# Kernel optimization log

Hardware: AMD Instinct MI355X
Metric: run time of the kernel (lower is better)

Reference implementation:

```python
import jax, jax.numpy as jnp
import numpy as np

# Config (matches BlockConfig defaults for linear attention)
B, S, D = 2, 4096, 2048
H, KVH, HD, CK = 16, 8, 128, 4   # n_heads, n_kv_heads, head_dim, conv_kernel
DQK, DV = KVH * HD, H * HD       # 1024, 2048
EPS = 1e-6


def setup_inputs() -> dict:
    key = jax.random.key(0)
    ks = jax.random.split(key, 12)
    std = 0.02
    return {
        "x": jax.random.normal(ks[0], (B, S, D), jnp.float32),
        "wq": jax.random.normal(ks[1], (DQK, D), jnp.float32) * std,
        "wk": jax.random.normal(ks[2], (DQK, D), jnp.float32) * std,
        "wv": jax.random.normal(ks[3], (DV, D), jnp.float32) * std,
        "wo": jax.random.normal(ks[4], (D, DV), jnp.float32) * std,
        "q_conv_w": jax.random.normal(ks[5], (DQK, 1, CK), jnp.float32) * std,
        "k_conv_w": jax.random.normal(ks[6], (DQK, 1, CK), jnp.float32) * std,
        "alpha_w": jax.random.normal(ks[7], (H, D), jnp.float32) * std,
        "alpha_b": jnp.zeros((H,), jnp.float32),
        "beta_w": jax.random.normal(ks[8], (H, D), jnp.float32) * std,
        "beta_b": jnp.zeros((H,), jnp.float32),
        "g_w": jax.random.normal(ks[9], (DV, D), jnp.float32) * std,
        "norm_q_w": jnp.ones((HD,), jnp.float32),
        "norm_k_w": jnp.ones((HD,), jnp.float32),
    }


def _rmsnorm(x, w):
    # normalize over last dim (head_dim) in fp32, elementwise affine, no bias
    xf = x.astype(jnp.float32)
    var = jnp.mean(xf * xf, axis=-1, keepdims=True)
    return (w * xf * jax.lax.rsqrt(var + EPS)).astype(x.dtype)


def _causal_dwconv(x, w):
    # x: (B, S, C); w: (C, 1, k) depthwise; torch Conv1d padding=k-1 then [:S]
    # == left-pad (k-1, 0) cross-correlation
    y = jax.lax.conv_general_dilated(
        x.transpose(0, 2, 1), w, window_strides=(1,),
        padding=[(CK - 1, 0)], feature_group_count=w.shape[0],
        dimension_numbers=("NCH", "OIH", "NCH"))
    return y.transpose(0, 2, 1)


def reference(x, wq, wk, wv, wo, q_conv_w, k_conv_w,
              alpha_w, alpha_b, beta_w, beta_b, g_w, norm_q_w, norm_k_w):
    Q = x @ wq.T                              # (B,S,DQK)
    K = x @ wk.T                              # (B,S,DQK)
    V = x @ wv.T                              # (B,S,DV)
    Q = _causal_dwconv(Q, q_conv_w)
    K = _causal_dwconv(K, k_conv_w)
    Q = _rmsnorm(Q.reshape(B, S, KVH, HD), norm_q_w)
    K = _rmsnorm(K.reshape(B, S, KVH, HD), norm_k_w)
    V = V.reshape(B, S, H, HD)
    alpha = jax.nn.sigmoid(x @ alpha_w.T + alpha_b)              # (B,S,H)
    beta = jax.nn.sigmoid(x @ beta_w.T + beta_b) / (HD ** 0.5)   # (B,S,H)
    rep = H // KVH
    Q = jnp.repeat(Q, rep, axis=2)            # (B,S,H,HD)
    K = jnp.repeat(K, rep, axis=2)

    # time-major for scan
    Qt = Q.transpose(1, 0, 2, 3)
    Kt = K.transpose(1, 0, 2, 3)
    Vt = V.transpose(1, 0, 2, 3)
    at = alpha.transpose(1, 0, 2)
    bt = beta.transpose(1, 0, 2)

    S0 = jnp.zeros((B, H, HD, HD), x.dtype)

    def step(S_state, inp):
        q_t, k_t, v_t, a_t, b_t = inp
        pred = jnp.einsum("bhd,bhdv->bhv", k_t, S_state)
        delta = v_t - pred
        update = jnp.einsum("bhv,bhd->bhdv", delta, k_t)
        S_state = a_t[:, :, None, None] * S_state + b_t[:, :, None, None] * update
        o_t = jnp.einsum("bhd,bhdv->bhv", q_t, S_state)
        return S_state, o_t

    _, O = jax.lax.scan(step, S0, (Qt, Kt, Vt, at, bt))  # O: (S,B,H,HD)
    out = O.transpose(1, 0, 2, 3).reshape(B, S, DV)
    g = jax.nn.sigmoid(x @ g_w.T)
    return (g * out) @ wo.T
```

## Files before the change

### kernel.cpp

```cpp
#include <hip/hip_runtime.h>
#include <stdint.h>

#define DEV static __device__ __forceinline__

typedef __bf16 bf16x8 __attribute__((ext_vector_type(8)));
typedef float f32x4 __attribute__((ext_vector_type(4)));

constexpr int Bc = 2, Sc = 4096, Dc = 2048, Hc = 16, KVHc = 8, HDc = 128;
constexpr int DQKc = 1024, DVc = 2048;
constexpr int Mc = Bc * Sc;
constexpr int NCATc = 6144;
constexpr int CT = 64;
constexpr int NCH = Sc / CT;
constexpr int COEF_STRIDE = 25088;
constexpr float EPSc = 1e-6f;

DEV uint16_t f2bf(float f) {
  uint32_t u = __float_as_uint(f);
  u += 0x7FFFu + ((u >> 16) & 1u);
  return (uint16_t)(u >> 16);
}
DEV float bf2f(uint16_t h) { return __uint_as_float(((uint32_t)h) << 16); }
DEV float sigmoidf_(float z) { return 1.0f / (1.0f + __expf(-z)); }

DEV void gload16(void* lds, const void* g) {
  auto gp = (const __attribute__((address_space(1))) uint32_t*)(uintptr_t)g;
  auto lp = (__attribute__((address_space(3))) uint32_t*)(uint32_t)(uintptr_t)lds;
  __builtin_amdgcn_global_load_lds(gp, lp, 16, 0, 0);
}

DEV void sync_lds() {
  asm volatile("s_waitcnt lgkmcnt(0)" ::: "memory");
  __builtin_amdgcn_sched_barrier(0);
  __builtin_amdgcn_s_barrier();
  __builtin_amdgcn_sched_barrier(0);
}

__global__ __launch_bounds__(256) void cast_kernel(const float* __restrict__ src,
                                                   uint16_t* __restrict__ dst, int n4) {
  int i = blockIdx.x * blockDim.x + threadIdx.x;
  int stride = gridDim.x * blockDim.x;
  for (; i < n4; i += stride) {
    float4 v = *(const float4*)(src + (size_t)i * 4);
    ushort4 o;
    o.x = f2bf(v.x); o.y = f2bf(v.y); o.z = f2bf(v.z); o.w = f2bf(v.w);
    *(ushort4*)(dst + (size_t)i * 4) = o;
  }
}

template <typename OutT>
__global__ __launch_bounds__(512, 2) void gemm256_bt(const uint16_t* __restrict__ A,
                                                     const uint16_t* __restrict__ Bw,
                                                     OutT* __restrict__ C, int Ndim, int Kdim,
                                                     int lda) {
  __shared__ uint16_t sT[2][2][2][8192];

  const int nbn = Ndim / 256;
  const int nwg = gridDim.x;
  int q = nwg >> 3, r = nwg & 7;
  int xcd = blockIdx.x & 7, lin = blockIdx.x >> 3;
  int swz = (xcd < r ? xcd * (q + 1) : r * (q + 1) + (xcd - r) * q) + lin;
  const int bm = swz / nbn, bn = swz % nbn;

  const int tid = threadIdx.x;
  const int wid = tid >> 6, lane = tid & 63;
  const int wm = wid >> 2, wn = wid & 3;
  const int lr = lane & 15;
  const int sswz8 = (((lane >> 4) ^ ((lr >> 1) & 3)) * 8);
  const int arow_base = wm * 128 + lr;
  const int brow_base = wn * 64 + lr;

  const uint16_t* Ab = A + (size_t)(bm * 256) * lda;
  const uint16_t* Bb = Bw + (size_t)(bn * 256) * Kdim;
  const int NT = Kdim >> 6;

  int srowA[2];
  int soff[2];
  const int wbase = tid & ~63;
#pragma unroll
  for (int u = 0; u < 2; ++u) {
    int L = u * 512 + tid;
    srowA[u] = L >> 2;
    soff[u] = (((L & 3) ^ ((L >> 3) & 3)) * 8);
  }

  auto STAGE = [&](int buf, int mat, int kh, int kt) {
    const uint16_t* gb = mat == 0 ? Ab : Bb;
    const int ld = mat == 0 ? lda : Kdim;
    uint16_t* rg = &sT[buf][mat][kh][0];
#pragma unroll
    for (int u = 0; u < 2; ++u) {
      const uint16_t* g = gb + (size_t)srowA[u] * ld + kt * 64 + kh * 32 + soff[u];
      gload16(rg + (u * 512 + wbase) * 8, g);
    }
  };

  f32x4 acc[8][4] = {};
  bf16x8 bfr[4];

  STAGE(0, 0, 0, 0); STAGE(0, 1, 0, 0);
  STAGE(0, 0, 1, 0); STAGE(0, 1, 1, 0);
  STAGE(1, 0, 0, 1); STAGE(1, 1, 0, 1);
  asm volatile("s_waitcnt vmcnt(4)" ::: "memory");
  __builtin_amdgcn_s_barrier();

  for (int kt = 0; kt < NT; ++kt) {
    const int buf = kt & 1;
    const uint16_t* aR0 = &sT[buf][0][0][0];
    const uint16_t* bR0 = &sT[buf][1][0][0];
    const uint16_t* aR1 = &sT[buf][0][1][0];
    const uint16_t* bR1 = &sT[buf][1][1][0];

    {
      bf16x8 af[4];
#pragma unroll
      for (int m = 0; m < 4; ++m)
        af[m] = *(const bf16x8*)&aR0[(arow_base + m * 16) * 32 + sswz8];
#pragma unroll
      for (int n = 0; n < 4; ++n)
        bfr[n] = *(const bf16x8*)&bR0[(brow_base + n * 16) * 32 + sswz8];
      if (kt + 1 < NT) STAGE(buf ^ 1, 0, 1, kt + 1);
      __builtin_amdgcn_s_setprio(1);
#pragma unroll
      for (int m = 0; m < 4; ++m)
#pragma unroll
        for (int n = 0; n < 4; ++n)
          acc[m][n] = __builtin_amdgcn_mfma_f32_16x16x32_bf16(af[m], bfr[n], acc[m][n], 0, 0, 0);
      __builtin_amdgcn_s_setprio(0);
      __builtin_amdgcn_s_barrier();
    }
    {
      bf16x8 af[4];
#pragma unroll
      for (int m = 0; m < 4; ++m)
        af[m] = *(const bf16x8*)&aR0[(arow_base + (m + 4) * 16) * 32 + sswz8];
      if (kt + 1 < NT) STAGE(buf ^ 1, 1, 1, kt + 1);
      __builtin_amdgcn_s_setprio(1);
#pragma unroll
      for (int m = 0; m < 4; ++m)
#pragma unroll
        for (int n = 0; n < 4; ++n)
          acc[m + 4][n] = __builtin_amdgcn_mfma_f32_16x16x32_bf16(af[m], bfr[n], acc[m + 4][n], 0, 0, 0);
      __builtin_amdgcn_s_setprio(0);
      __builtin_amdgcn_s_barrier();
    }
    {
      bf16x8 af[4];
#pragma unroll
      for (int m = 0; m < 4; ++m)
        af[m] = *(const bf16x8*)&aR1[(arow_base + m * 16) * 32 + sswz8];
#pragma unroll
      for (int n = 0; n < 4; ++n)
        bfr[n] = *(const bf16x8*)&bR1[(brow_base + n * 16) * 32 + sswz8];
      if (kt + 2 < NT) STAGE(buf, 0, 0, kt + 2);
      __builtin_amdgcn_s_setprio(1);
#pragma unroll
      for (int m = 0; m < 4; ++m)
#pragma unroll
        for (int n = 0; n < 4; ++n)
          acc[m][n] = __builtin_amdgcn_mfma_f32_16x16x32_bf16(af[m], bfr[n], acc[m][n], 0, 0, 0);
      __builtin_amdgcn_s_setprio(0);
      __builtin_amdgcn_s_barrier();
    }
    {
      bf16x8 af[4];
#pragma unroll
      for (int m = 0; m < 4; ++m)
        af[m] = *(const bf16x8*)&aR1[(arow_base + (m + 4) * 16) * 32 + sswz8];
      if (kt + 2 < NT) STAGE(buf, 1, 0, kt + 2);
      __builtin_amdgcn_s_setprio(1);
#pragma unroll
      for (int m = 0; m < 4; ++m)
#pragma unroll
        for (int n = 0; n < 4; ++n)
          acc[m + 4][n] = __builtin_amdgcn_mfma_f32_16x16x32_bf16(af[m], bfr[n], acc[m + 4][n], 0, 0, 0);
      __builtin_amdgcn_s_setprio(0);
    }
    if (kt + 1 < NT) {
      if (kt + 2 < NT)
        asm volatile("s_waitcnt vmcnt(4)" ::: "memory");
      else
        asm volatile("s_waitcnt vmcnt(0)" ::: "memory");
      __builtin_amdgcn_s_barrier();
    }
  }

  const int r0 = (lane >> 4) * 4;
#pragma unroll
  for (int m = 0; m < 8; ++m)
#pragma unroll
    for (int n = 0; n < 4; ++n) {
      int col = bn * 256 + wn * 64 + n * 16 + lr;
#pragma unroll
      for (int j = 0; j < 4; ++j) {
        int row = bm * 256 + wm * 128 + m * 16 + r0 + j;
        float val = acc[m][n][j];
        if constexpr (sizeof(OutT) == 2)
          C[(size_t)row * Ndim + col] = (OutT)f2bf(val);
        else
          C[(size_t)row * Ndim + col] = (OutT)val;
      }
    }
}

__global__ __launch_bounds__(256) void alphabeta_kernel(const float* __restrict__ x,
                                                        const float* __restrict__ aw,
                                                        const float* __restrict__ abias,
                                                        const float* __restrict__ bw,
                                                        const float* __restrict__ bbias,
                                                        float* __restrict__ out) {
  __shared__ float xs[4 * Dc];
  const int row0 = blockIdx.x * 4;
  const float* xp = x + (size_t)row0 * Dc;
  for (int i = threadIdx.x; i < 4 * Dc / 4; i += 256)
    *(float4*)&xs[i * 4] = *(const float4*)(xp + (size_t)i * 4);
  __syncthreads();
  const int o = threadIdx.x >> 3, lg = threadIdx.x & 7;
  const float* wrow = (o < 16) ? (aw + (size_t)o * Dc) : (bw + (size_t)(o - 16) * Dc);
  float s0 = 0.f, s1 = 0.f, s2 = 0.f, s3 = 0.f;
  for (int k = lg * 4; k < Dc; k += 32) {
    float4 wv = *(const float4*)(wrow + k);
    float4 x0 = *(const float4*)&xs[k];
    float4 x1 = *(const float4*)&xs[Dc + k];
    float4 x2 = *(const float4*)&xs[2 * Dc + k];
    float4 x3 = *(const float4*)&xs[3 * Dc + k];
    s0 += x0.x * wv.x + x0.y * wv.y + x0.z * wv.z + x0.w * wv.w;
    s1 += x1.x * wv.x + x1.y * wv.y + x1.z * wv.z + x1.w * wv.w;
    s2 += x2.x * wv.x + x2.y * wv.y + x2.z * wv.z + x2.w * wv.w;
    s3 += x3.x * wv.x + x3.y * wv.y + x3.z * wv.z + x3.w * wv.w;
  }
#pragma unroll
  for (int m = 1; m < 8; m <<= 1) {
    s0 += __shfl_xor(s0, m); s1 += __shfl_xor(s1, m);
    s2 += __shfl_xor(s2, m); s3 += __shfl_xor(s3, m);
  }
  if (lg == 0) {
    float bias = (o < 16) ? abias[o] : bbias[o - 16];
    float scale = (o >= 16) ? 0.08838834764831845f : 1.0f;
    out[(size_t)(row0 + 0) * 32 + o] = sigmoidf_(s0 + bias) * scale;
    out[(size_t)(row0 + 1) * 32 + o] = sigmoidf_(s1 + bias) * scale;
    out[(size_t)(row0 + 2) * 32 + o] = sigmoidf_(s2 + bias) * scale;
    out[(size_t)(row0 + 3) * 32 + o] = sigmoidf_(s3 + bias) * scale;
  }
}

__global__ __launch_bounds__(256) void convnorm_kernel(const uint16_t* __restrict__ C1,
                                                       const float* __restrict__ qcw,
                                                       const float* __restrict__ kcw,
                                                       const float* __restrict__ nqw,
                                                       const float* __restrict__ nkw,
                                                       uint16_t* __restrict__ Qn,
                                                       uint16_t* __restrict__ Kn) {
  const int wid = blockIdx.x * 4 + (threadIdx.x >> 6);
  const int lane = threadIdx.x & 63;
  const int kvh = wid & 7;
  const int t = (wid >> 3) & (Sc - 1);
  const int b = wid >> 15;
  float qv[2], kv[2];
#pragma unroll
  for (int half = 0; half < 2; ++half) {
    const int c = lane + half * 64;
    const int ch = kvh * HDc + c;
    float qs = 0.f, ks = 0.f;
#pragma unroll
    for (int j = 0; j < 4; ++j) {
      int tt = t - 3 + j;
      if (tt >= 0) {
        size_t rb = (size_t)(b * Sc + tt) * NCATc;
        qs = fmaf(bf2f(C1[rb + ch]), qcw[ch * 4 + j], qs);
        ks = fmaf(bf2f(C1[rb + 1024 + ch]), kcw[ch * 4 + j], ks);
      }
    }
    qv[half] = qs; kv[half] = ks;
  }
  float sq = qv[0] * qv[0] + qv[1] * qv[1];
  float sk = kv[0] * kv[0] + kv[1] * kv[1];
#pragma unroll
  for (int m = 1; m < 64; m <<= 1) { sq += __shfl_xor(sq, m); sk += __shfl_xor(sk, m); }
  const float rq = rsqrtf(sq * (1.f / HDc) + EPSc);
  const float rk = rsqrtf(sk * (1.f / HDc) + EPSc);
#pragma unroll
  for (int half = 0; half < 2; ++half) {
    const int c = lane + half * 64;
    size_t oidx = (size_t)(b * Sc + t) * DQKc + kvh * HDc + c;
    Qn[oidx] = f2bf(nqw[c] * qv[half] * rq);
    Kn[oidx] = f2bf(nkw[c] * kv[half] * rk);
  }
}

__global__ __launch_bounds__(256) void scores_kernel(const uint16_t* __restrict__ Qn,
                                                     const uint16_t* __restrict__ Kn,
                                                     const float* __restrict__ ab,
                                                     uint8_t* __restrict__ coef) {
  __shared__ __align__(16) char smem[137728];
  uint16_t* sK = (uint16_t*)smem;
  uint16_t* sQ = (uint16_t*)(smem + 17408);
  uint16_t* sF = (uint16_t*)smem;
  uint16_t* sM2 = (uint16_t*)(smem + 18432);
  float* Lb = (float*)(smem + 108544);
  float* bbv = Lb + 128;
  uint16_t* Ktg = (uint16_t*)(smem + 109568);
  uint16_t* Et = (uint16_t*)(smem + 128000);
  float* gCb = (float*)(smem + 137216);

  auto Wt_p  = [&](int hd) { return (float*)(smem + hd * 17408); };
  auto Msh_p = [&](int hd) { return (uint16_t*)(smem + 34816 + hd * 18432); };
  auto Msl_p = [&](int hd) { return (uint16_t*)(smem + 44032 + hd * 18432); };
  auto Thh_p = [&](int hd) { return (uint16_t*)(smem + 71680 + hd * 18432); };
  auto Thl_p = [&](int hd) { return (uint16_t*)(smem + 80896 + hd * 18432); };

  const int bid = blockIdx.x;
  const int c = bid & 63, kh = (bid >> 6) & 7, b = bid >> 9;
  const int t0 = c * 64;
  const int tid = threadIdx.x;
  const int w = tid >> 6, l = tid & 63, lr = l & 15, lk = (l >> 4) * 8;
  const int sr = tid >> 2, sq2 = tid & 3;

  auto cb_p = [&](int hd) {
    return coef + (size_t)((b * Hc + kh * 2 + hd) * NCH + c) * COEF_STRIDE;
  };

  {
    const size_t rb = (size_t)(b * Sc + t0 + sr) * DQKc + kh * HDc + sq2 * 32;
#pragma unroll
    for (int u = 0; u < 4; ++u) {
      uint4 kv = *(const uint4*)(Kn + rb + u * 8);
      uint4 qv = *(const uint4*)(Qn + rb + u * 8);
      *(uint4*)&sK[sr * 136 + sq2 * 32 + u * 8] = kv;
      *(uint4*)&sQ[sr * 136 + sq2 * 32 + u * 8] = qv;
    }
  }
  if (tid < 128) {
    const int hd = tid >> 6, tt = tid & 63;
    const float* abp = ab + (size_t)(b * Sc + t0 + tt) * 32 + (kh * 2 + hd);
    float av = fmaxf(abp[0], 1e-30f);
    float bv = abp[16];
    float la = log2f(av);
    float L = la;
#pragma unroll
    for (int off = 1; off < 64; off <<= 1) {
      float up = __shfl_up(L, off, 64);
      if (tt >= off) L += up;
    }
    Lb[hd * 64 + tt] = L; bbv[hd * 64 + tt] = bv;
    float* gout = (float*)(cb_p(hd) + 24576);
    gout[tt] = exp2f(L - la);
    gout[64 + tt] = exp2f(L);
  }
  __syncthreads();

  f32x4 kkacc[4] = {}, qkacc[4] = {};
#pragma unroll
  for (int k0 = 0; k0 < 128; k0 += 32) {
    bf16x8 ka = *(const bf16x8*)&sK[(16 * w + lr) * 136 + k0 + lk];
    bf16x8 qa = *(const bf16x8*)&sQ[(16 * w + lr) * 136 + k0 + lk];
#pragma unroll
    for (int n = 0; n < 4; ++n) {
      bf16x8 kb = *(const bf16x8*)&sK[(16 * n + lr) * 136 + k0 + lk];
      kkacc[n] = __builtin_amdgcn_mfma_f32_16x16x32_bf16(ka, kb, kkacc[n], 0, 0, 0);
      qkacc[n] = __builtin_amdgcn_mfma_f32_16x16x32_bf16(qa, kb, qkacc[n], 0, 0, 0);
    }
  }
  __syncthreads();

  {
#pragma unroll
    for (int u = 0; u < 4; ++u) {
      uint4 kd = *(const uint4*)&sK[sr * 136 + sq2 * 32 + u * 8];
      const int c0 = sq2 * 32 + u * 8;
      const int tsw = sr ^ (sq2 << 4);
      uint32_t x0 = kd.x, x1 = kd.y, x2 = kd.z, x3 = kd.w;
      Ktg[(c0 + 0) * 72 + tsw] = (uint16_t)x0; Ktg[(c0 + 1) * 72 + tsw] = (uint16_t)(x0 >> 16);
      Ktg[(c0 + 2) * 72 + tsw] = (uint16_t)x1; Ktg[(c0 + 3) * 72 + tsw] = (uint16_t)(x1 >> 16);
      Ktg[(c0 + 4) * 72 + tsw] = (uint16_t)x2; Ktg[(c0 + 5) * 72 + tsw] = (uint16_t)(x2 >> 16);
      Ktg[(c0 + 6) * 72 + tsw] = (uint16_t)x3; Ktg[(c0 + 7) * 72 + tsw] = (uint16_t)(x3 >> 16);
    }
    if (tid < 128) {
      const int hd = tid >> 6, tt = tid & 63;
      gCb[hd * 64 + tt] = exp2f(Lb[hd * 64 + 63] - Lb[hd * 64 + tt]) * bbv[hd * 64 + tt];
    }
  }
  __syncthreads();

#pragma unroll
  for (int hd = 0; hd < 2; ++hd) {
    float* Wt = Wt_p(hd);
    uint16_t* Mh = Msh_p(hd);
    uint16_t* Ml = Msl_p(hd);
    const float* Lh = Lb + hd * 64;
    const float* bh = bbv + hd * 64;
#pragma unroll
    for (int n = 0; n < 4; ++n)
#pragma unroll
      for (int jj = 0; jj < 4; ++jj) {
        const int i = 16 * w + (l >> 4) * 4 + jj;
        const int j = 16 * n + lr;
        float Li = Lh[i];
        float Lim = (i > 0) ? Lh[(i > 0) ? i - 1 : 0] : 0.f;
        float Lj = Lh[j];
        float bj = bh[j];
        float wv = (j < i) ? exp2f(Lim - Lj) * bj * kkacc[n][jj] : 0.f;
        Wt[j * 68 + i] = wv;
        float ms = (j <= i) ? exp2f(Li - Lj) * bj * qkacc[n][jj] : 0.f;
        uint16_t mh = f2bf(ms);
        Mh[i * 72 + j] = mh;
        Ml[i * 72 + j] = f2bf(ms - bf2f(mh));
      }
  }
  __syncthreads();

  if (tid < 128) {
    const int hd = tid >> 6, col = tid & 63;
    float* Wt = Wt_p(hd);
    uint16_t* Th = Thh_p(hd);
    uint16_t* Tl = Thl_p(hd);
    float acc[64];
#pragma unroll
    for (int i = 0; i < 64; ++i) acc[i] = 0.f;
#pragma unroll
    for (int ll = 0; ll < 64; ++ll) {
      float xl = ((col == ll) ? 1.f : 0.f) - acc[ll];
      uint16_t xh = f2bf(xl);
      Th[col * 72 + ll] = xh;
      Tl[col * 72 + ll] = f2bf(xl - bf2f(xh));
#pragma unroll
      for (int i = ll + 1; i < 64; ++i)
        acc[i] = fmaf(Wt[ll * 68 + i], xl, acc[i]);
    }
  }
  __syncthreads();

  for (int hd = 0; hd < 2; ++hd) {
    uint16_t* Mh = Msh_p(hd);
    uint16_t* Ml = Msl_p(hd);
    uint16_t* Th = Thh_p(hd);
    uint16_t* Tl = Thl_p(hd);
    uint16_t* m2out = (uint16_t*)cb_p(hd);
    uint16_t* fout = (uint16_t*)cb_p(hd) + 4096;

    {
      const int j2 = tid >> 2, tq = tid & 3;
#pragma unroll
      for (int p = 0; p < 16; ++p) {
        int t1 = tq * 16 + p;
        float ev = gCb[hd * 64 + t1] * (bf2f(Th[j2 * 72 + t1]) + bf2f(Tl[j2 * 72 + t1]));
        Et[j2 * 72 + t1] = f2bf(ev);
      }
    }
    __syncthreads();

    f32x4 m2acc[4] = {};
#pragma unroll
    for (int k0 = 0; k0 < 64; k0 += 32) {
      bf16x8 ah = *(const bf16x8*)&Mh[(16 * w + lr) * 72 + k0 + lk];
      bf16x8 al = *(const bf16x8*)&Ml[(16 * w + lr) * 72 + k0 + lk];
#pragma unroll
      for (int n = 0; n < 4; ++n) {
        bf16x8 bhf = *(const bf16x8*)&Th[(16 * n + lr) * 72 + k0 + lk];
        bf16x8 blf = *(const bf16x8*)&Tl[(16 * n + lr) * 72 + k0 + lk];
        m2acc[n] = __builtin_amdgcn_mfma_f32_16x16x32_bf16(ah, bhf, m2acc[n], 0, 0, 0);
        m2acc[n] = __builtin_amdgcn_mfma_f32_16x16x32_bf16(ah, blf, m2acc[n], 0, 0, 0);
        m2acc[n] = __builtin_amdgcn_mfma_f32_16x16x32_bf16(al, bhf, m2acc[n], 0, 0, 0);
      }
    }
    f32x4 facc[2][4] = {};
#pragma unroll
    for (int k0 = 0; k0 < 64; k0 += 32) {
      bf16x8 eb[4];
#pragma unroll
      for (int n = 0; n < 4; ++n)
        eb[n] = *(const bf16x8*)&Et[(16 * n + lr) * 72 + k0 + lk];
      const int ksw = (k0 + lk) ^ (w << 4);
      bf16x8 ka0 = *(const bf16x8*)&Ktg[(32 * w + lr) * 72 + ksw];
      bf16x8 ka1 = *(const bf16x8*)&Ktg[(32 * w + 16 + lr) * 72 + ksw];
#pragma unroll
      for (int n = 0; n < 4; ++n) {
        facc[0][n] = __builtin_amdgcn_mfma_f32_16x16x32_bf16(ka0, eb[n], facc[0][n], 0, 0, 0);
        facc[1][n] = __builtin_amdgcn_mfma_f32_16x16x32_bf16(ka1, eb[n], facc[1][n], 0, 0, 0);
      }
    }
#pragma unroll
    for (int n = 0; n < 4; ++n)
#pragma unroll
      for (int jj = 0; jj < 4; ++jj) {
        const int i = 16 * w + (l >> 4) * 4 + jj;
        const int j = 16 * n + lr;
        sM2[i * 72 + j] = f2bf(m2acc[n][jj]);
        sF[(32 * w + (l >> 4) * 4 + jj) * 72 + j] = f2bf(facc[0][n][jj]);
        sF[(32 * w + 16 + (l >> 4) * 4 + jj) * 72 + j] = f2bf(facc[1][n][jj]);
      }
    __syncthreads();
    {
      const int i2 = tid >> 2, tq = tid & 3;
      uint4 a0 = *(const uint4*)&sM2[i2 * 72 + tq * 16];
      uint4 a1 = *(const uint4*)&sM2[i2 * 72 + tq * 16 + 8];
      *(uint4*)(m2out + i2 * 64 + tq * 16) = a0;
      *(uint4*)(m2out + i2 * 64 + tq * 16 + 8) = a1;
#pragma unroll
      for (int e = 0; e < 4; ++e) {
        int L = tid * 4 + e;
        int rw = L >> 3, cu = (L & 7) * 8;
        *(uint4*)(fout + rw * 64 + cu) = *(const uint4*)&sF[rw * 72 + cu];
      }
    }
    __syncthreads();
  }
}

__global__ __launch_bounds__(256) void scan_kernel(const uint16_t* __restrict__ Qn,
                                                   const uint16_t* __restrict__ Kn,
                                                   uint16_t* C1,
                                                   const uint8_t* __restrict__ coef) {
  __shared__ __align__(16) uint16_t Kb[64 * 136];
  __shared__ __align__(16) uint16_t Qb[64 * 136];
  __shared__ __align__(16) uint16_t M2b[64 * 72];
  __shared__ __align__(16) uint16_t Fb[128 * 72];
  __shared__ __align__(16) uint16_t Vb[64 * 24];
  __shared__ __align__(16) uint16_t Rt[16 * 72];
  __shared__ __align__(16) uint16_t Sh[16 * 136];
  __shared__ __align__(16) uint16_t Slo[16 * 136];
  __shared__ float gABb[128];

  const int bid = blockIdx.x;
  const int kh = bid & 7;
  const int j2 = bid >> 3;
  const int sl = j2 >> 2;
  const int b = (j2 >> 1) & 1;
  const int h = kh * 2 + (j2 & 1);
  const int ch0 = (b * Hc + h) * NCH;

  const int tid = threadIdx.x;
  const int w = tid >> 6, l = tid & 63;
  const int lr = l & 15, lk = (l >> 4) * 8;
  const int row0 = 16 * w + (l >> 4) * 4;
  const int vcol = lr;
  const int sr = tid >> 2, sq2 = tid & 3;

  const size_t kqbase = (size_t)(b * Sc) * DQKc + kh * HDc;
  const size_t vbase = (size_t)(b * Sc) * NCATc + 2048 + h * HDc + sl * 16;
  uint16_t* Gb = C1 + (size_t)(b * Sc) * NCATc + 4096 + h * HDc + sl * 16 + vcol;

  float sreg[2][4] = {};
  uint4 kA[4], kB[4], qA[4], qB[4];
  ushort4 gv0, gv1;

  auto LOADS = [&](int cn, uint4 (&kd)[4], uint4 (&qd)[4], uint4 (&m2d)[2], uint4 (&fd)[4],
                   uint4& vd, float& gd, ushort4& gvd) {
    const size_t rb = kqbase + (size_t)(cn * CT + sr) * DQKc + sq2 * 32;
#pragma unroll
    for (int u = 0; u < 4; ++u) {
      kd[u] = *(const uint4*)(Kn + rb + u * 8);
      qd[u] = *(const uint4*)(Qn + rb + u * 8);
    }
    const uint16_t* cf = (const uint16_t*)(coef + (size_t)(ch0 + cn) * COEF_STRIDE);
#pragma unroll
    for (int e = 0; e < 2; ++e)
      m2d[e] = *(const uint4*)(cf + sr * 64 + sq2 * 16 + e * 8);
#pragma unroll
    for (int e = 0; e < 4; ++e)
      fd[e] = *(const uint4*)(cf + 4096 + (tid * 4 + e) * 8);
    if (tid < 128) {
      vd = *(const uint4*)(C1 + vbase + (size_t)(cn * CT + (tid >> 1)) * NCATc + (tid & 1) * 8);
      gd = ((const float*)(cf + 12288))[tid];
    }
    const uint16_t* gpre = Gb + (size_t)(cn * CT) * NCATc;
    gvd.x = gpre[(size_t)(row0 + 0) * NCATc];
    gvd.y = gpre[(size_t)(row0 + 1) * NCATc];
    gvd.z = gpre[(size_t)(row0 + 2) * NCATc];
    gvd.w = gpre[(size_t)(row0 + 3) * NCATc];
  };
  auto WSTAGE = [&](const uint4 (&kd)[4], const uint4 (&qd)[4], const uint4 (&m2d)[2],
                    const uint4 (&fd)[4], const uint4& vd, const float& gd) {
#pragma unroll
    for (int u = 0; u < 4; ++u) {
      *(uint4*)&Kb[sr * 136 + sq2 * 32 + u * 8] = kd[u];
      *(uint4*)&Qb[sr * 136 + sq2 * 32 + u * 8] = qd[u];
    }
#pragma unroll
    for (int e = 0; e < 2; ++e)
      *(uint4*)&M2b[sr * 72 + sq2 * 16 + e * 8] = m2d[e];
#pragma unroll
    for (int e = 0; e < 4; ++e) {
      int L = tid * 4 + e;
      *(uint4*)&Fb[(L >> 3) * 72 + (L & 7) * 8] = fd[e];
    }
    if (tid < 128) {
      *(uint4*)&Vb[(tid >> 1) * 24 + (tid & 1) * 8] = vd;
      gABb[tid] = gd;
    }
  };

  auto CHUNK = [&](int c, bool pre, uint4 (&kcur)[4], uint4 (&knxt)[4],
                   uint4 (&qcur)[4], uint4 (&qnxt)[4], ushort4& gvcur, ushort4& gvnxt) {
    uint4 m2d[2], fd[4]; uint4 vd; float gd = 0.f;
    if (pre) LOADS(c + 1, knxt, qnxt, m2d, fd, vd, gd, gvnxt);

    f32x4 accP = {0, 0, 0, 0}, accPq = {0, 0, 0, 0};
#pragma unroll
    for (int k0 = 0; k0 < 128; k0 += 32) {
      bf16x8 ka = *(const bf16x8*)&Kb[(16 * w + lr) * 136 + k0 + lk];
      bf16x8 qa = *(const bf16x8*)&Qb[(16 * w + lr) * 136 + k0 + lk];
      bf16x8 shf = *(const bf16x8*)&Sh[lr * 136 + k0 + lk];
      bf16x8 slf = *(const bf16x8*)&Slo[lr * 136 + k0 + lk];
      accP = __builtin_amdgcn_mfma_f32_16x16x32_bf16(ka, shf, accP, 0, 0, 0);
      accP = __builtin_amdgcn_mfma_f32_16x16x32_bf16(ka, slf, accP, 0, 0, 0);
      accPq = __builtin_amdgcn_mfma_f32_16x16x32_bf16(qa, shf, accPq, 0, 0, 0);
      accPq = __builtin_amdgcn_mfma_f32_16x16x32_bf16(qa, slf, accPq, 0, 0, 0);
    }
    float gbv[4];
#pragma unroll
    for (int j = 0; j < 4; ++j) gbv[j] = gABb[64 + row0 + j];
    const float gT = gABb[127];
    {
      float rv[4];
#pragma unroll
      for (int j = 0; j < 4; ++j) {
        float vv = bf2f(Vb[(row0 + j) * 24 + vcol]);
        float ga = gABb[row0 + j];
        rv[j] = vv - ga * accP[j];
      }
      uint32_t r01 = (uint32_t)f2bf(rv[0]) | ((uint32_t)f2bf(rv[1]) << 16);
      uint32_t r23 = (uint32_t)f2bf(rv[2]) | ((uint32_t)f2bf(rv[3]) << 16);
      *(uint2*)&Rt[vcol * 72 + row0] = make_uint2(r01, r23);
    }
    sync_lds();

    f32x4 accO = {0, 0, 0, 0};
    f32x4 accY0 = {0, 0, 0, 0}, accY1 = {0, 0, 0, 0};
#pragma unroll
    for (int k0 = 0; k0 < 64; k0 += 32) {
      bf16x8 rb8 = *(const bf16x8*)&Rt[lr * 72 + k0 + lk];
      bf16x8 ma = *(const bf16x8*)&M2b[(16 * w + lr) * 72 + k0 + lk];
      bf16x8 f0 = *(const bf16x8*)&Fb[(32 * w + lr) * 72 + k0 + lk];
      bf16x8 f1 = *(const bf16x8*)&Fb[(32 * w + 16 + lr) * 72 + k0 + lk];
      accO = __builtin_amdgcn_mfma_f32_16x16x32_bf16(ma, rb8, accO, 0, 0, 0);
      accY0 = __builtin_amdgcn_mfma_f32_16x16x32_bf16(f0, rb8, accY0, 0, 0, 0);
      accY1 = __builtin_amdgcn_mfma_f32_16x16x32_bf16(f1, rb8, accY1, 0, 0, 0);
    }
    {
      uint16_t* gp = Gb + (size_t)(c * CT) * NCATc;
      uint16_t gvv[4] = {gvcur.x, gvcur.y, gvcur.z, gvcur.w};
#pragma unroll
      for (int j = 0; j < 4; ++j) {
        float o = gbv[j] * accPq[j] + accO[j];
        float gg = sigmoidf_(bf2f(gvv[j]));
        gp[(size_t)(row0 + j) * NCATc] = f2bf(o * gg);
      }
    }
    {
      uint16_t hi[4], lo[4];
#pragma unroll
      for (int j = 0; j < 4; ++j) {
        float s = gT * sreg[0][j] + accY0[j];
        sreg[0][j] = s;
        hi[j] = f2bf(s);
        lo[j] = f2bf(s - bf2f(hi[j]));
      }
      const int dk0 = 32 * w + (l >> 4) * 4;
      *(uint2*)&Sh[vcol * 136 + dk0] =
          make_uint2((uint32_t)hi[0] | ((uint32_t)hi[1] << 16),
                     (uint32_t)hi[2] | ((uint32_t)hi[3] << 16));
      *(uint2*)&Slo[vcol * 136 + dk0] =
          make_uint2((uint32_t)lo[0] | ((uint32_t)lo[1] << 16),
                     (uint32_t)lo[2] | ((uint32_t)lo[3] << 16));
    }
    {
      uint16_t hi[4], lo[4];
#pragma unroll
      for (int j = 0; j < 4; ++j) {
        float s = gT * sreg[1][j] + accY1[j];
        sreg[1][j] = s;
        hi[j] = f2bf(s);
        lo[j] = f2bf(s - bf2f(hi[j]));
      }
      const int dk0 = 32 * w + 16 + (l >> 4) * 4;
      *(uint2*)&Sh[vcol * 136 + dk0] =
          make_uint2((uint32_t)hi[0] | ((uint32_t)hi[1] << 16),
                     (uint32_t)hi[2] | ((uint32_t)hi[3] << 16));
      *(uint2*)&Slo[vcol * 136 + dk0] =
          make_uint2((uint32_t)lo[0] | ((uint32_t)lo[1] << 16),
                     (uint32_t)lo[2] | ((uint32_t)lo[3] << 16));
    }
    if (pre) WSTAGE(knxt, qnxt, m2d, fd, vd, gd);
    sync_lds();
  };

  {
    uint4 m2d[2], fd[4]; uint4 vd; float gd = 0.f;
    LOADS(0, kA, qA, m2d, fd, vd, gd, gv0);
    WSTAGE(kA, qA, m2d, fd, vd, gd);
  }
  for (int i = tid; i < 16 * 136; i += 256) { Sh[i] = 0; Slo[i] = 0; }
  __syncthreads();

  for (int c2 = 0; c2 < NCH; c2 += 2) {
    CHUNK(c2, true, kA, kB, qA, qB, gv0, gv1);
    CHUNK(c2 + 1, c2 + 2 < NCH, kB, kA, qB, qA, gv1, gv0);
  }
}

extern "C" void kernel_launch(void* const* d_in, const int* in_sizes, int n_in,
                              void* d_out, int out_size, void* d_ws, size_t ws_size,
                              hipStream_t stream) {
  (void)in_sizes; (void)n_in; (void)out_size; (void)ws_size;
  const float* x     = (const float*)d_in[0];
  const float* wq    = (const float*)d_in[1];
  const float* wk    = (const float*)d_in[2];
  const float* wv    = (const float*)d_in[3];
  const float* wo    = (const float*)d_in[4];
  const float* qcw   = (const float*)d_in[5];
  const float* kcw   = (const float*)d_in[6];
  const float* aw    = (const float*)d_in[7];
  const float* abias = (const float*)d_in[8];
  const float* bw    = (const float*)d_in[9];
  const float* bbias = (const float*)d_in[10];
  const float* gw    = (const float*)d_in[11];
  const float* nqw   = (const float*)d_in[12];
  const float* nkw   = (const float*)d_in[13];

  uint8_t* ws = (uint8_t*)d_ws;
  uint16_t* xb   = (uint16_t*)(ws);
  uint16_t* wcat = (uint16_t*)(ws + 33554432);
  uint16_t* wob  = (uint16_t*)(ws + 58720256);
  uint16_t* c1   = (uint16_t*)(ws + 67108864);
  float*    abuf = (float*)   (ws + 167772160);
  uint16_t* qn   = (uint16_t*)(ws + 168820736);
  uint16_t* kn   = (uint16_t*)(ws + 185597952);
  uint8_t*  cofs = (uint8_t*)ws;

  cast_kernel<<<2048, 256, 0, stream>>>(x, xb, Mc * Dc / 4);
  cast_kernel<<<1024, 256, 0, stream>>>(wq, wcat, DQKc * Dc / 4);
  cast_kernel<<<1024, 256, 0, stream>>>(wk, wcat + DQKc * Dc, DQKc * Dc / 4);
  cast_kernel<<<1024, 256, 0, stream>>>(wv, wcat + 2 * DQKc * Dc, DVc * Dc / 4);
  cast_kernel<<<1024, 256, 0, stream>>>(gw, wcat + 2 * DQKc * Dc + DVc * Dc, DVc * Dc / 4);
  cast_kernel<<<1024, 256, 0, stream>>>(wo, wob, DVc * Dc / 4);

  gemm256_bt<uint16_t><<<768, 512, 0, stream>>>(xb, wcat, c1, NCATc, Dc, Dc);
  alphabeta_kernel<<<2048, 256, 0, stream>>>(x, aw, abias, bw, bbias, abuf);
  convnorm_kernel<<<16384, 256, 0, stream>>>(c1, qcw, kcw, nqw, nkw, qn, kn);
  scores_kernel<<<1024, 256, 0, stream>>>(qn, kn, abuf, cofs);
  scan_kernel<<<256, 256, 0, stream>>>(qn, kn, c1, cofs);
  gemm256_bt<float><<<256, 512, 0, stream>>>(c1 + 4096, wob, (float*)d_out, DVc, Dc, NCATc);
}
```

Before: 852.8 us.

## Load scan coefficients directly into double-buffered swizzled LDS via async global loads

The producer kernel now writes the M2 and F coefficient tiles in an XOR-swizzled layout. The scan kernel fetches them straight into double-buffered LDS with gload16 (global-to-LDS) instead of staging through registers and writing them back. This is meant to cut register pressure and the VGPR-to-LDS store traffic on the serial chunk loop, and the swizzle avoids bank conflicts without padding. The cost is more LDS for the double buffers and a switch to a full __syncthreads, which has to cover completion of the async loads. Launch bounds now set occupancy to 1.

Result: faster. 710.3 us (-16.7%).

```diff
diff --git a/kernel.cpp b/kernel.cpp
--- a/kernel.cpp
+++ b/kernel.cpp
@@ -494,27 +494,27 @@
       const int i2 = tid >> 2, tq = tid & 3;
       uint4 a0 = *(const uint4*)&sM2[i2 * 72 + tq * 16];
       uint4 a1 = *(const uint4*)&sM2[i2 * 72 + tq * 16 + 8];
-      *(uint4*)(m2out + i2 * 64 + tq * 16) = a0;
-      *(uint4*)(m2out + i2 * 64 + tq * 16 + 8) = a1;
+      *(uint4*)(m2out + i2 * 64 + ((2 * tq) ^ (i2 & 7)) * 8) = a0;
+      *(uint4*)(m2out + i2 * 64 + ((2 * tq + 1) ^ (i2 & 7)) * 8) = a1;
 #pragma unroll
       for (int e = 0; e < 4; ++e) {
         int L = tid * 4 + e;
-        int rw = L >> 3, cu = (L & 7) * 8;
-        *(uint4*)(fout + rw * 64 + cu) = *(const uint4*)&sF[rw * 72 + cu];
+        int rw = L >> 3, s = L & 7;
+        *(uint4*)(fout + rw * 64 + (s ^ (rw & 7)) * 8) = *(const uint4*)&sF[rw * 72 + s * 8];
       }
     }
     __syncthreads();
   }
 }
 
-__global__ __launch_bounds__(256) void scan_kernel(const uint16_t* __restrict__ Qn,
-                                                   const uint16_t* __restrict__ Kn,
-                                                   uint16_t* C1,
-                                                   const uint8_t* __restrict__ coef) {
+__global__ __launch_bounds__(256, 1) void scan_kernel(const uint16_t* __restrict__ Qn,
+                                                      const uint16_t* __restrict__ Kn,
+                                                      uint16_t* C1,
+                                                      const uint8_t* __restrict__ coef) {
   __shared__ __align__(16) uint16_t Kb[64 * 136];
   __shared__ __align__(16) uint16_t Qb[64 * 136];
-  __shared__ __align__(16) uint16_t M2b[64 * 72];
-  __shared__ __align__(16) uint16_t Fb[128 * 72];
+  __shared__ __align__(16) uint16_t M2b[2][64 * 64];
+  __shared__ __align__(16) uint16_t Fb[2][128 * 64];
   __shared__ __align__(16) uint16_t Vb[64 * 24];
   __shared__ __align__(16) uint16_t Rt[16 * 72];
   __shared__ __align__(16) uint16_t Sh[16 * 136];
@@ -535,6 +535,7 @@
   const int row0 = 16 * w + (l >> 4) * 4;
   const int vcol = lr;
   const int sr = tid >> 2, sq2 = tid & 3;
+  const int wbase = tid & ~63;
 
   const size_t kqbase = (size_t)(b * Sc) * DQKc + kh * HDc;
   const size_t vbase = (size_t)(b * Sc) * NCATc + 2048 + h * HDc + sl * 16;
@@ -544,21 +545,21 @@
   uint4 kA[4], kB[4], qA[4], qB[4];
   ushort4 gv0, gv1;
 
-  auto LOADS = [&](int cn, uint4 (&kd)[4], uint4 (&qd)[4], uint4 (&m2d)[2], uint4 (&fd)[4],
+  auto LOADS = [&](int cn, int nb, uint4 (&kd)[4], uint4 (&qd)[4],
                    uint4& vd, float& gd, ushort4& gvd) {
+    const uint16_t* cf = (const uint16_t*)(coef + (size_t)(ch0 + cn) * COEF_STRIDE);
+#pragma unroll
+    for (int u = 0; u < 2; ++u)
+      gload16(&M2b[nb][(u * 256 + wbase) * 8], cf + (size_t)(u * 256 + tid) * 8);
+#pragma unroll
+    for (int u = 0; u < 4; ++u)
+      gload16(&Fb[nb][(u * 256 + wbase) * 8], cf + 4096 + (size_t)(u * 256 + tid) * 8);
     const size_t rb = kqbase + (size_t)(cn * CT + sr) * DQKc + sq2 * 32;
 #pragma unroll
     for (int u = 0; u < 4; ++u) {
       kd[u] = *(const uint4*)(Kn + rb + u * 8);
       qd[u] = *(const uint4*)(Qn + rb + u * 8);
     }
-    const uint16_t* cf = (const uint16_t*)(coef + (size_t)(ch0 + cn) * COEF_STRIDE);
-#pragma unroll
-    for (int e = 0; e < 2; ++e)
-      m2d[e] = *(const uint4*)(cf + sr * 64 + sq2 * 16 + e * 8);
-#pragma unroll
-    for (int e = 0; e < 4; ++e)
-      fd[e] = *(const uint4*)(cf + 4096 + (tid * 4 + e) * 8);
     if (tid < 128) {
       vd = *(const uint4*)(C1 + vbase + (size_t)(cn * CT + (tid >> 1)) * NCATc + (tid & 1) * 8);
       gd = ((const float*)(cf + 12288))[tid];
@@ -569,21 +570,13 @@
     gvd.z = gpre[(size_t)(row0 + 2) * NCATc];
     gvd.w = gpre[(size_t)(row0 + 3) * NCATc];
   };
-  auto WSTAGE = [&](const uint4 (&kd)[4], const uint4 (&qd)[4], const uint4 (&m2d)[2],
-                    const uint4 (&fd)[4], const uint4& vd, const float& gd) {
+  auto WSTAGE = [&](const uint4 (&kd)[4], const uint4 (&qd)[4],
+                    const uint4& vd, const float& gd) {
 #pragma unroll
     for (int u = 0; u < 4; ++u) {
       *(uint4*)&Kb[sr * 136 + sq2 * 32 + u * 8] = kd[u];
       *(uint4*)&Qb[sr * 136 + sq2 * 32 + u * 8] = qd[u];
     }
-#pragma unroll
-    for (int e = 0; e < 2; ++e)
-      *(uint4*)&M2b[sr * 72 + sq2 * 16 + e * 8] = m2d[e];
-#pragma unroll
-    for (int e = 0; e < 4; ++e) {
-      int L = tid * 4 + e;
-      *(uint4*)&Fb[(L >> 3) * 72 + (L & 7) * 8] = fd[e];
-    }
     if (tid < 128) {
       *(uint4*)&Vb[(tid >> 1) * 24 + (tid & 1) * 8] = vd;
       gABb[tid] = gd;
@@ -592,8 +585,9 @@
 
   auto CHUNK = [&](int c, bool pre, uint4 (&kcur)[4], uint4 (&knxt)[4],
                    uint4 (&qcur)[4], uint4 (&qnxt)[4], ushort4& gvcur, ushort4& gvnxt) {
-    uint4 m2d[2], fd[4]; uint4 vd; float gd = 0.f;
-    if (pre) LOADS(c + 1, knxt, qnxt, m2d, fd, vd, gd, gvnxt);
+    uint4 vd; float gd = 0.f;
+    if (pre) LOADS(c + 1, (c + 1) & 1, knxt, qnxt, vd, gd, gvnxt);
+    const int cb = c & 1;
 
     f32x4 accP = {0, 0, 0, 0}, accPq = {0, 0, 0, 0};
 #pragma unroll
@@ -629,10 +623,11 @@
     f32x4 accY0 = {0, 0, 0, 0}, accY1 = {0, 0, 0, 0};
 #pragma unroll
     for (int k0 = 0; k0 < 64; k0 += 32) {
+      const int sw = ((((k0 >> 3) + (l >> 4)) ^ (lr & 7)) * 8);
       bf16x8 rb8 = *(const bf16x8*)&Rt[lr * 72 + k0 + lk];
-      bf16x8 ma = *(const bf16x8*)&M2b[(16 * w + lr) * 72 + k0 + lk];
-      bf16x8 f0 = *(const bf16x8*)&Fb[(32 * w + lr) * 72 + k0 + lk];
-      bf16x8 f1 = *(const bf16x8*)&Fb[(32 * w + 16 + lr) * 72 + k0 + lk];
+      bf16x8 ma = *(const bf16x8*)&M2b[cb][(16 * w + lr) * 64 + sw];
+      bf16x8 f0 = *(const bf16x8*)&Fb[cb][(32 * w + lr) * 64 + sw];
+      bf16x8 f1 = *(const bf16x8*)&Fb[cb][(32 * w + 16 + lr) * 64 + sw];
       accO = __builtin_amdgcn_mfma_f32_16x16x32_bf16(ma, rb8, accO, 0, 0, 0);
       accY0 = __builtin_amdgcn_mfma_f32_16x16x32_bf16(f0, rb8, accY0, 0, 0, 0);
       accY1 = __builtin_amdgcn_mfma_f32_16x16x32_bf16(f1, rb8, accY1, 0, 0, 0);
@@ -681,14 +676,14 @@
           make_uint2((uint32_t)lo[0] | ((uint32_t)lo[1] << 16),
                      (uint32_t)lo[2] | ((uint32_t)lo[3] << 16));
     }
-    if (pre) WSTAGE(knxt, qnxt, m2d, fd, vd, gd);
-    sync_lds();
+    if (pre) WSTAGE(knxt, qnxt, vd, gd);
+    __syncthreads();
   };
 
   {
-    uint4 m2d[2], fd[4]; uint4 vd; float gd = 0.f;
-    LOADS(0, kA, qA, m2d, fd, vd, gd, gv0);
-    WSTAGE(kA, qA, m2d, fd, vd, gd);
+    uint4 vd; float gd = 0.f;
+    LOADS(0, 0, kA, qA, vd, gd, gv0);
+    WSTAGE(kA, qA, vd, gd);
   }
   for (int i = tid; i < 16 * 136; i += 256) { Sh[i] = 0; Slo[i] = 0; }
   __syncthreads();
```
